# Kernel optimization log

Hardware: AMD Instinct MI355X
Metric: run time of the kernel (lower is better)

Reference implementation:

```python
import jax, jax.numpy as jnp
import numpy as np


def _ln(x, w, b, eps=1e-5):
    m = x.mean(-1, keepdims=True)
    v = jnp.mean((x - m) ** 2, axis=-1, keepdims=True)
    return (x - m) * jax.lax.rsqrt(v + eps) * w + b


def _to_seq(xc, g):
    # xc: [B,Di,H,W] -> [B,L,Di]; g0: row-major fwd, g1: row-major rev,
    # g2: col-major fwd, g3: col-major rev (CrossScan_1..4)
    if g >= 2:
        xc = xc.transpose(0, 1, 3, 2)
    s = xc.reshape(xc.shape[0], xc.shape[1], -1)
    if g % 2 == 1:
        s = jnp.flip(s, -1)
    return s.transpose(0, 2, 1)


def _from_seq(y, g, H, W):
    # y: [B,L,Di] -> [B,H,W,Di], inverse of _to_seq (CrossMerge_1..4)
    if g % 2 == 1:
        y = jnp.flip(y, 1)
    Bn, L, Di = y.shape
    if g >= 2:
        return y.reshape(Bn, W, H, Di).transpose(0, 2, 1, 3)
    return y.reshape(Bn, H, W, Di)


def _sscan(dA, dBx, Cm):
    # selective scan: h_t = dA_t*h + dBx_t ; y_t = <h_t, C_t>
    # dA,dBx: [B,L,Di,S], Cm: [B,L,S] -> y: [B,L,Di]
    def step(h, inp):
        a, bx, c = inp
        h = a * h + bx
        return h, jnp.einsum('bds,bs->bd', h, c)
    h0 = jnp.zeros(dA.shape[:1] + dA.shape[2:], dA.dtype)
    _, ys = jax.lax.scan(step, h0, (dA.transpose(1, 0, 2, 3), dBx.transpose(1, 0, 2, 3), Cm.transpose(1, 0, 2)))
    return ys.transpose(1, 0, 2)


def _ss2d(xc, g, H, W, ipw, ipb, cw, cb, xpw, dtw, dtb, A_log, Ds, onw, onb, opw, opb):
    R = dtw.shape[-1]
    S = A_log.shape[-1]
    xz = xc @ ipw.T + ipb                      # [B,H,W,2*Di]
    Di = xz.shape[-1] // 2
    xi, z = xz[..., :Di], xz[..., Di:]
    xi = xi.transpose(0, 3, 1, 2)              # [B,Di,H,W]
    xi = jax.lax.conv_general_dilated(xi, cw, (1, 1), [(1, 1), (1, 1)],
                                      dimension_numbers=('NCHW', 'OIHW', 'NCHW'),
                                      feature_group_count=Di) + cb[None, :, None, None]
    xi = jax.nn.silu(xi)
    seq = _to_seq(xi, g)                       # [B,L,Di]
    xdbl = seq @ xpw.T                         # [B,L,R+2S]
    dtr, Bm, Cm = xdbl[..., :R], xdbl[..., R:R + S], xdbl[..., R + S:]
    dt = jax.nn.softplus(dtr @ dtw.T + dtb)    # [B,L,Di]
    A = -jnp.exp(A_log)                        # [Di,S]
    dA = jnp.exp(dt[..., None] * A)            # [B,L,Di,S]
    dBx = (dt * seq)[..., None] * Bm[:, :, None, :]
    y = _sscan(dA, dBx, Cm) + Ds * seq
    y = _from_seq(y, g, H, W)                  # [B,H,W,Di]
    y = _ln(y, onw, onb)
    y = y * jax.nn.silu(z)
    return y @ opw.T + opb


def setup_inputs() -> dict:
    Bn, Hh, Ww, C = 8, 96, 96, 256
    Di = C // 4
    S = 1
    R = max(1, (Di + 15) // 16)
    key = jax.random.key(0)
    ks = jax.random.split(key, 12)
    nrm = lambda k, sh, s: jax.random.normal(k, sh, jnp.float32) * s
    return {
        'x': nrm(ks[0], (Bn, Hh * Ww, C), 1.0),
        'norm_w': jnp.ones((C,), jnp.float32), 'norm_b': jnp.zeros((C,), jnp.float32),
        'fc_w': nrm(ks[1], (C, C), 0.02), 'fc_b': jnp.zeros((C,), jnp.float32),
        'conv1d_w': nrm(ks[2], (1, 1, 3), 0.3),
        'in_proj_w': nrm(ks[3], (4, 2 * Di, Di), 0.05), 'in_proj_b': jnp.zeros((4, 2 * Di), jnp.float32),
        'conv2d_w': nrm(ks[4], (4, Di, 1, 3, 3), 0.2), 'conv2d_b': jnp.zeros((4, Di), jnp.float32),
        'x_proj_w': nrm(ks[5], (4, R + 2 * S, Di), 0.05),
        'dt_w': nrm(ks[6], (4, Di, R), 0.1), 'dt_b': nrm(ks[7], (4, Di), 0.1),
        'A_log': nrm(ks[8], (4, Di, S), 0.1),
        'Ds': jnp.ones((4, Di), jnp.float32),
        'out_norm_w': jnp.ones((4, Di), jnp.float32), 'out_norm_b': jnp.zeros((4, Di), jnp.float32),
        'out_proj_w': nrm(ks[9], (4, Di, Di), 0.05), 'out_proj_b': jnp.zeros((4, Di), jnp.float32),
        'proj_w': nrm(ks[10], (C, C), 0.02), 'proj_b': jnp.zeros((C,), jnp.float32),
        'skip_scale': jnp.ones((1,), jnp.float32),
        'H': Hh, 'W': Ww,
    }


def reference(x, norm_w, norm_b, fc_w, fc_b, conv1d_w, in_proj_w, in_proj_b, conv2d_w, conv2d_b,
              x_proj_w, dt_w, dt_b, A_log, Ds, out_norm_w, out_norm_b, out_proj_w, out_proj_b,
              proj_w, proj_b, skip_scale, H, W):
    B, N, C = x.shape
    xn = _ln(x, norm_w, norm_b)
    z_avg = xn.mean(1)                         # [B,C] (permute(0,2,1).mean(2))
    yg = jax.lax.conv_general_dilated(z_avg[:, None, :], conv1d_w, (1,), [(1, 1)],
                                      dimension_numbers=('NCH', 'OIH', 'NCH'))[:, 0, :]
    gate = jax.nn.sigmoid(z_avg @ fc_w.T + fc_b + yg)   # fc_out_2 [B,C]
    xg = xn.reshape(B, H, W, C)
    Dg = C // 4
    outs = [_ss2d(xg[..., g * Dg:(g + 1) * Dg], g, H, W,
                  in_proj_w[g], in_proj_b[g], conv2d_w[g], conv2d_b[g], x_proj_w[g],
                  dt_w[g], dt_b[g], A_log[g], Ds[g], out_norm_w[g], out_norm_b[g],
                  out_proj_w[g], out_proj_b[g]) for g in range(4)]
    xm = jnp.concatenate(outs, -1) * skip_scale * xg
    xm = xm.reshape(B, N, C) * gate[:, None, :]
    xm = _ln(xm, norm_w, norm_b)
    return xm @ proj_w.T + proj_b
```

## Files before the change

### kernel.cpp

```cpp
#include <hip/hip_runtime.h>
#include <math.h>

#define HH 96
#define WWI 96
#define NN 9216
#define CC 256
#define LL 9216
#define CHK 96
#define NCH 96
#define BB 8
#define BN (BB*NN)

__device__ __forceinline__ float softplusf(float x){
    float e = expf(-fabsf(x));
    return fmaxf(x, 0.f) + log1pf(e);
}
__device__ __forceinline__ float sigmf(float x){ return 1.f / (1.f + expf(-x)); }

__device__ __forceinline__ float wredsum(float v){
    #pragma unroll
    for(int o = 32; o > 0; o >>= 1) v += __shfl_xor(v, o, 64);
    return v;
}

__device__ __forceinline__ void wredsum2(float& s, float& q){
    #pragma unroll
    for(int o = 32; o > 0; o >>= 1){
        s += __shfl_xor(s, o, 64);
        q += __shfl_xor(q, o, 64);
    }
}

__device__ __forceinline__ void chunk_walk(int g, int chunk, int& base, int& step){
    if(g == 0){ base = chunk * 96;        step = 1;   }
    else if(g == 1){ base = 9215 - chunk * 96; step = -1; }
    else if(g == 2){ base = chunk;        step = 96;  }
    else { base = 9215 - chunk;           step = -96; }
}

__global__ __launch_bounds__(256) void k_stats(const float* __restrict__ x,
                                               float* __restrict__ mrs){
    int wid = threadIdx.x >> 6, lane = threadIdx.x & 63;
    size_t row = (size_t)blockIdx.x * 4 + wid;
    float4 v = ((const float4*)(x + row * CC))[lane];
    float s = wredsum(v.x + v.y + v.z + v.w);
    float q = wredsum(v.x*v.x + v.y*v.y + v.z*v.z + v.w*v.w);
    float m = s * (1.f/256.f);
    float var = q * (1.f/256.f) - m*m;
    float rs = rsqrtf(fmaxf(var, 0.f) + 1e-5f);
    if(lane == 0){ mrs[2*row] = m; mrs[2*row+1] = rs; }
}

__global__ __launch_bounds__(256) void k_prew(const float* __restrict__ pw,
        const float* __restrict__ nw, const float* __restrict__ nb,
        const float* __restrict__ pb, float* __restrict__ Wn,
        float* __restrict__ wsum, float* __restrict__ cvec){
    int o = threadIdx.x;
    float ws = 0.f, cc = 0.f;
    for(int k = 0; k < 256; k++){
        float w = pw[(size_t)o * 256 + k];
        float wn = w * nw[k];
        Wn[(size_t)o * 256 + k] = wn;
        ws += wn; cc += w * nb[k];
    }
    wsum[o] = ws; cvec[o] = cc + pb[o];
}

__global__ __launch_bounds__(128) void k_prewip(const float* __restrict__ ipw,
        const float* __restrict__ nw, const float* __restrict__ nb,
        const float* __restrict__ ipb, float* __restrict__ Wip,
        float* __restrict__ wsip, float* __restrict__ cvip){
    int g = blockIdx.x, o = threadIdx.x;
    const float* wr = ipw + ((size_t)(g*128 + o)) * 64;
    float ws = 0.f, cc = 0.f;
    for(int k = 0; k < 64; k++){
        float w = wr[k];
        float wn = w * nw[g*64 + k];
        Wip[((size_t)(g*128 + o))*64 + k] = wn;
        ws += wn; cc += w * nb[g*64 + k];
    }
    wsip[g*128 + o] = ws;
    cvip[g*128 + o] = cc + ipb[g*128 + o];
}

__global__ __launch_bounds__(256) void k_zavg(const float* __restrict__ x,
        const float* __restrict__ mrs, const float* __restrict__ nw,
        const float* __restrict__ nb, float* __restrict__ zpart){
    int c = threadIdx.x, b = blockIdx.y, t0 = blockIdx.x * 256;
    float nwv = nw[c], nbv = nb[c];
    float s = 0.f;
    for(int i = 0; i < 256; i++){
        size_t r = (size_t)b * NN + t0 + i;
        s += (x[r * CC + c] - mrs[2*r]) * mrs[2*r+1] * nwv + nbv;
    }
    zpart[((size_t)b * 36 + blockIdx.x) * CC + c] = s;
}

__global__ __launch_bounds__(256) void k_gate(const float* __restrict__ zpart,
        const float* __restrict__ fcw, const float* __restrict__ fcb,
        const float* __restrict__ w1d, float* __restrict__ gate){
    __shared__ float za[CC];
    int c = threadIdx.x, b = blockIdx.x;
    float s = 0.f;
    for(int t = 0; t < 36; t++) s += zpart[((size_t)b * 36 + t) * CC + c];
    za[c] = s * (1.f/(float)NN);
    __syncthreads();
    float zm1 = (c > 0)     ? za[c-1] : 0.f;
    float zp1 = (c < CC-1)  ? za[c+1] : 0.f;
    float acc = fcb[c] + w1d[0]*zm1 + w1d[1]*za[c] + w1d[2]*zp1;
    const float* wr = fcw + (size_t)c * CC;
    for(int k = 0; k < CC; k++) acc += za[k] * wr[k];
    gate[b * CC + c] = sigmf(acc);
}

__global__ __launch_bounds__(256) void k_inproj2(const float* __restrict__ x,
        const float* __restrict__ mrs, const float* __restrict__ Wip,
        const float* __restrict__ wsip, const float* __restrict__ cvip,
        float* __restrict__ xib, float* __restrict__ zbuf){
    int t = threadIdx.x;
    int g = blockIdx.y * 2 + (t >> 7);
    int h = (t >> 6) & 1;
    int c = t & 63;
    int r0 = blockIdx.x * 16;
    int b  = r0 / NN;
    int n0 = r0 - b * NN;
    int oc = g*128 + h*64 + c;
    float wv[64];
    {
        const float4* wr = (const float4*)(Wip + (size_t)oc * 64);
        #pragma unroll
        for(int j = 0; j < 16; j++){
            float4 t4 = wr[j];
            wv[4*j+0] = t4.x; wv[4*j+1] = t4.y;
            wv[4*j+2] = t4.z; wv[4*j+3] = t4.w;
        }
    }
    float acc[16];
    const float* ab = x + (size_t)r0 * CC + g * 64;
    #pragma unroll 4
    for(int r = 0; r < 16; r++){
        const float4* ar = (const float4*)(ab + (size_t)r * CC);
        float s0 = 0.f, s1 = 0.f;
        #pragma unroll
        for(int j = 0; j < 8; j++){
            float4 u = ar[j], v = ar[j + 8];
            s0 += u.x*wv[4*j+0]  + u.y*wv[4*j+1]  + u.z*wv[4*j+2]  + u.w*wv[4*j+3];
            s1 += v.x*wv[32+4*j] + v.y*wv[33+4*j] + v.z*wv[34+4*j] + v.w*wv[35+4*j];
        }
        acc[r] = s0 + s1;
    }
    float ws = wsip[oc], cv = cvip[oc];
    size_t obase = ((size_t)(b*4 + g)) * NN + n0;
    #pragma unroll
    for(int r = 0; r < 16; r++){
        size_t row = (size_t)r0 + r;
        float m = mrs[2*row], rs = mrs[2*row+1];
        float v = rs * acc[r] - m * rs * ws + cv;
        if(h == 0)
            xib[(obase + r)*64 + c] = v;
        else
            zbuf[(obase + r)*64 + c] = v * sigmf(v);
    }
}

__global__ __launch_bounds__(256) void k_inproj(const float* __restrict__ x,
        const float* __restrict__ mrs, const float* __restrict__ nw,
        const float* __restrict__ nb, const float* __restrict__ ipw,
        const float* __restrict__ ipb, float* __restrict__ xib,
        float* __restrict__ zbuf){
    int tile = blockIdx.x, b = blockIdx.y, g = blockIdx.z;
    int n0 = tile * 128;
    __shared__ float xs[128 * 64];
    int tid = threadIdx.x;
    for(int idx = tid; idx < 2048; idx += 256){
        int p = idx >> 4, k4 = (idx & 15) * 4;
        size_t r = (size_t)b * NN + n0 + p;
        float4 v = *(const float4*)(x + r * CC + g*64 + k4);
        float m = mrs[2*r], rs = mrs[2*r+1];
        float4 w4 = *(const float4*)(nw + g*64 + k4);
        float4 b4 = *(const float4*)(nb + g*64 + k4);
        float4 o;
        o.x = (v.x - m)*rs*w4.x + b4.x;
        o.y = (v.y - m)*rs*w4.y + b4.y;
        o.z = (v.z - m)*rs*w4.z + b4.z;
        o.w = (v.w - m)*rs*w4.w + b4.w;
        *(float4*)(xs + p*64 + k4) = o;
    }
    __syncthreads();
    int c = tid & 63, ph = tid >> 6;
    float wx[64], wz[64];
    {
        const float* wrx = ipw + ((size_t)(g*128 + c)) * 64;
        const float* wrz = ipw + ((size_t)(g*128 + 64 + c)) * 64;
        #pragma unroll
        for(int k = 0; k < 64; k++){ wx[k] = wrx[k]; wz[k] = wrz[k]; }
    }
    float bx = ipb[g*128 + c], bz = ipb[g*128 + 64 + c];
    size_t obase = ((size_t)(b*4 + g)) * NN + n0;
    for(int p = ph*32; p < ph*32 + 32; p++){
        const float4* xp = (const float4*)(xs + p*64);
        float a0 = 0.f, a1 = 0.f, z0 = 0.f, z1 = 0.f;
        #pragma unroll
        for(int k4 = 0; k4 < 16; k4 += 2){
            float4 u = xp[k4], v = xp[k4+1];
            a0 += u.x*wx[4*k4+0]; a1 += u.y*wx[4*k4+1];
            a0 += u.z*wx[4*k4+2]; a1 += u.w*wx[4*k4+3];
            z0 += u.x*wz[4*k4+0]; z1 += u.y*wz[4*k4+1];
            z0 += u.z*wz[4*k4+2]; z1 += u.w*wz[4*k4+3];
            a0 += v.x*wx[4*k4+4]; a1 += v.y*wx[4*k4+5];
            a0 += v.z*wx[4*k4+6]; a1 += v.w*wx[4*k4+7];
            z0 += v.x*wz[4*k4+4]; z1 += v.y*wz[4*k4+5];
            z0 += v.z*wz[4*k4+6]; z1 += v.w*wz[4*k4+7];
        }
        float xv = bx + a0 + a1;
        float zv = bz + z0 + z1;
        xib[(obase + p)*64 + c] = xv;
        zbuf[(obase + p)*64 + c] = zv * sigmf(zv);
    }
}

__global__ __launch_bounds__(256) void k_conv(const float* __restrict__ xib,
        const float* __restrict__ cw, const float* __restrict__ cb,
        float* __restrict__ out){
    int tile = blockIdx.x, b = blockIdx.y, g = blockIdx.z;
    int h0 = (tile/12)*8, w0 = (tile%12)*8;
    __shared__ float xs[100*64];
    int tid = threadIdx.x;
    size_t ibase = ((size_t)(b*4+g)) * NN;
    for(int i = tid; i < 6400; i += 256){
        int p = i >> 6, k = i & 63;
        int ph = h0 + p/10 - 1, pw = w0 + p%10 - 1;
        float v = 0.f;
        if(ph >= 0 && ph < HH && pw >= 0 && pw < WWI)
            v = xib[(ibase + (size_t)(ph*WWI + pw))*64 + k];
        xs[i] = v;
    }
    __syncthreads();
    int c = tid & 63, q = tid >> 6;
    float wk[9];
    const float* wp = cw + ((size_t)(g*64 + c))*9;
    #pragma unroll
    for(int j = 0; j < 9; j++) wk[j] = wp[j];
    float bias2 = cb[g*64 + c];
    for(int pi = q*16; pi < q*16+16; pi++){
        int py = pi >> 3, px = pi & 7;
        float acc = bias2;
        #pragma unroll
        for(int dy = 0; dy < 3; dy++)
            #pragma unroll
            for(int dx = 0; dx < 3; dx++)
                acc += xs[((py+dy)*10 + px+dx)*64 + c] * wk[dy*3+dx];
        float sv = acc * sigmf(acc);
        size_t r = (size_t)b*NN + (h0+py)*WWI + (w0+px);
        out[r*CC + g*64 + c] = sv;
    }
}

template<int ZPRE>
__global__ __launch_bounds__(256) void k_ipconv(const float* __restrict__ x,
        const float* __restrict__ mrs, const float* __restrict__ nw,
        const float* __restrict__ nb, const float* __restrict__ ipw,
        const float* __restrict__ ipb, const float* __restrict__ cw,
        const float* __restrict__ cb, float* __restrict__ out,
        float* __restrict__ zbuf){
    int tile = blockIdx.x, b = blockIdx.y, g = blockIdx.z;
    int h0 = (tile / 12) * 8, w0 = (tile % 12) * 8;
    __shared__ float xs[100 * 64];
    __shared__ float xi[100 * 64];
    int tid = threadIdx.x;
    for(int i = tid; i < 6400; i += 256){
        int p = i >> 6, k = i & 63;
        int ph = h0 + p / 10 - 1, pw = w0 + p % 10 - 1;
        float v = 0.f;
        if(ph >= 0 && ph < HH && pw >= 0 && pw < WWI){
            size_t r = (size_t)b * NN + ph * WWI + pw;
            v = (x[r * CC + g*64 + k] - mrs[2*r]) * mrs[2*r+1]
                * nw[g*64 + k] + nb[g*64 + k];
        }
        xs[i] = v;
    }
    __syncthreads();
    int c = tid & 63, q = tid >> 6;
    {
        float wv[64];
        const float* wr = ipw + ((size_t)(g * 128 + c)) * 64;
        #pragma unroll
        for(int k = 0; k < 64; k++) wv[k] = wr[k];
        float bias = ipb[g * 128 + c];
        for(int p = q * 25; p < q * 25 + 25; p++){
            int ph = h0 + p / 10 - 1, pw = w0 + p % 10 - 1;
            bool valid = (ph >= 0 && ph < HH && pw >= 0 && pw < WWI);
            float acc = bias;
            const float* xp = &xs[p * 64];
            #pragma unroll
            for(int k = 0; k < 64; k++) acc += xp[k] * wv[k];
            xi[p * 64 + c] = valid ? acc : 0.f;
        }
    }
    __syncthreads();
    float wk[9];
    const float* wp = cw + ((size_t)(g * 64 + c)) * 9;
    #pragma unroll
    for(int j = 0; j < 9; j++) wk[j] = wp[j];
    float bias2 = cb[g * 64 + c];
    for(int pi = q * 16; pi < q * 16 + 16; pi++){
        int py = pi >> 3, px = pi & 7;
        float acc = bias2;
        #pragma unroll
        for(int dy = 0; dy < 3; dy++)
            #pragma unroll
            for(int dx = 0; dx < 3; dx++)
                acc += xi[((py + dy) * 10 + px + dx) * 64 + c] * wk[dy*3 + dx];
        float sv = acc * sigmf(acc);
        size_t r = (size_t)b * NN + (h0 + py) * WWI + (w0 + px);
        out[r * CC + g*64 + c] = sv;
    }
    if(ZPRE){
        float wzv[64];
        const float* wr = ipw + ((size_t)(g * 128 + 64 + c)) * 64;
        #pragma unroll
        for(int k = 0; k < 64; k++) wzv[k] = wr[k];
        float zbv = ipb[g * 128 + 64 + c];
        size_t zb0 = ((size_t)(b * 4 + g)) * NN;
        for(int p16 = 0; p16 < 16; p16++){
            int p = q * 16 + p16;
            int py = p >> 3, px = p & 7;
            const float* xp = &xs[((py + 1) * 10 + (px + 1)) * 64];
            float acc = zbv;
            #pragma unroll
            for(int k = 0; k < 64; k++) acc += xp[k] * wzv[k];
            zbuf[(zb0 + (size_t)((h0 + py) * WWI + (w0 + px))) * 64 + c]
                = acc * sigmf(acc);
        }
    }
}

__global__ __launch_bounds__(64) void k_scan1(const float* __restrict__ out,
        const float* __restrict__ xpw, const float* __restrict__ dtw,
        const float* __restrict__ dtb, const float* __restrict__ alog,
        float* __restrict__ ap_out, float* __restrict__ h_out){
    int chunk = blockIdx.x, gb = blockIdx.y;
    int g = gb >> 3, b = gb & 7, d = threadIdx.x;
    __shared__ float s_seq[CHK * 65];
    __shared__ float s_xd[CHK * 6];
    __shared__ float s_w[6 * 64];
    int base, step; chunk_walk(g, chunk, base, step);
    const float* xg = out + (size_t)b * NN * CC + g * 64;
    for(int j = 0; j < CHK; j++)
        s_seq[j * 65 + d] = xg[(size_t)(base + j * step) * CC + d];
    for(int i = d; i < 384; i += 64) s_w[i] = xpw[g * 384 + i];
    __syncthreads();
    for(int idx = d; idx < CHK*6; idx += 64){
        int l = idx / 6, j = idx % 6;
        float acc = 0.f;
        const float* sr = &s_seq[l * 65];
        const float* wr = &s_w[j * 64];
        #pragma unroll
        for(int k = 0; k < 64; k++) acc += sr[k] * wr[k];
        s_xd[idx] = acc;
    }
    __syncthreads();
    int gd = g * 64 + d;
    float Av = -expf(alog[gd]);
    float db = dtb[gd];
    float w0 = dtw[gd*4], w1 = dtw[gd*4+1], w2 = dtw[gd*4+2], w3 = dtw[gd*4+3];
    float h = 0.f, apd = 1.f;
    #pragma unroll 4
    for(int l = 0; l < CHK; l++){
        const float* xd = &s_xd[l * 6];
        float xv = s_seq[l*65 + d];
        float dt = softplusf(xd[0]*w0 + xd[1]*w1 + xd[2]*w2 + xd[3]*w3 + db);
        float a = expf(dt * Av);
        h = a*h + dt*xv*xd[4];
        apd *= a;
    }
    int ob = (gb * NCH + chunk) * 64 + d;
    ap_out[ob] = apd; h_out[ob] = h;
}

__global__ __launch_bounds__(256) void k_scan2(const float* __restrict__ ap,
        const float* __restrict__ he, float* __restrict__ hinit){
    int idx = blockIdx.x * 256 + threadIdx.x;
    int gb = idx >> 6, d = idx & 63;
    float h = 0.f;
    for(int c = 0; c < NCH; c++){
        int o = (gb * NCH + c) * 64 + d;
        hinit[o] = h;
        h = ap[o]*h + he[o];
    }
}

template<int ZPRE>
__global__ __launch_bounds__(64) void k_scan3(float* __restrict__ out,
        const float* __restrict__ x, const float* __restrict__ mrs,
        const float* __restrict__ nw, const float* __restrict__ nb,
        const float* __restrict__ ipw, const float* __restrict__ ipb,
        const float* __restrict__ xpw, const float* __restrict__ dtw,
        const float* __restrict__ dtb, const float* __restrict__ alog,
        const float* __restrict__ Dsp, const float* __restrict__ onw,
        const float* __restrict__ onb, const float* __restrict__ hinit,
        const float* __restrict__ zbuf){
    int chunk = blockIdx.x, gb = blockIdx.y;
    int g = gb >> 3, b = gb & 7, d = threadIdx.x;
    __shared__ float s_seq[CHK * 65];
    __shared__ float s_xd[CHK * 6];
    __shared__ float s_w[6 * 64];
    __shared__ float xnt[(ZPRE ? 1 : CHK) * 65];
    int base, step; chunk_walk(g, chunk, base, step);
    float* xg = out + (size_t)b * NN * CC + g * 64;
    for(int j = 0; j < CHK; j++)
        s_seq[j * 65 + d] = xg[(size_t)(base + j * step) * CC + d];
    if(!ZPRE){
        float nwv = nw[g*64 + d], nbv = nb[g*64 + d];
        for(int j = 0; j < CHK; j++){
            int n = base + j * step;
            size_t r = (size_t)b * NN + n;
            xnt[j * 65 + d] = (x[r * CC + g*64 + d] - mrs[2*r]) * mrs[2*r+1] * nwv + nbv;
        }
    }
    for(int i = d; i < 384; i += 64) s_w[i] = xpw[g * 384 + i];
    __syncthreads();
    for(int idx = d; idx < CHK*6; idx += 64){
        int l = idx / 6, j = idx % 6;
        float acc = 0.f;
        const float* sr = &s_seq[l * 65];
        const float* wr = &s_w[j * 64];
        #pragma unroll
        for(int k = 0; k < 64; k++) acc += sr[k] * wr[k];
        s_xd[idx] = acc;
    }
    __syncthreads();
    int gd = g * 64 + d;
    float Av = -expf(alog[gd]);
    float db = dtb[gd];
    float Dv = Dsp[gd];
    float w0 = dtw[gd*4], w1 = dtw[gd*4+1], w2 = dtw[gd*4+2], w3 = dtw[gd*4+3];
    float h = hinit[(gb * NCH + chunk) * 64 + d];
    #pragma unroll 4
    for(int l = 0; l < CHK; l++){
        const float* xd = &s_xd[l * 6];
        float xv = s_seq[l*65 + d];
        float dt = softplusf(xd[0]*w0 + xd[1]*w1 + xd[2]*w2 + xd[3]*w3 + db);
        float a = expf(dt * Av);
        h = a*h + dt*xv*xd[4];
        s_seq[l*65 + d] = h * xd[5] + Dv * xv;
    }
    float wON = onw[gd], bON = onb[gd];
    float wz[ZPRE ? 1 : 64];
    float zb = 0.f;
    if(!ZPRE){
        const float* wr = ipw + ((size_t)(g * 128 + 64 + d)) * 64;
        #pragma unroll
        for(int k = 0; k < 64; k++) wz[k] = wr[k];
        zb = ipb[g * 128 + 64 + d];
    }
    const float* zp = zbuf + (((size_t)(b * 4 + g)) * NN) * 64 + d;
    #pragma unroll 4
    for(int l = 0; l < CHK; l++){
        float y = s_seq[l*65 + d];
        float s = y, q = y * y;
        wredsum2(s, q);
        float m = s * (1.f/64.f);
        float var = q * (1.f/64.f) - m*m;
        float rs = rsqrtf(fmaxf(var, 0.f) + 1e-5f);
        float lny = (y - m) * rs * wON + bON;
        int n = base + l * step;
        float zs;
        if(ZPRE){
            zs = zp[(size_t)n * 64];
        } else {
            float z = zb;
            const float* xp = &xnt[l * 65];
            #pragma unroll
            for(int k = 0; k < 64; k++) z += xp[k] * wz[k];
            zs = z * sigmf(z);
        }
        xg[(size_t)n * CC + d] = lny * zs;
    }
}

__global__ __launch_bounds__(64) void k_out2(float* __restrict__ out,
        const float* __restrict__ x, const float* __restrict__ mrs,
        const float* __restrict__ nw, const float* __restrict__ nb,
        const float* __restrict__ opw, const float* __restrict__ opb,
        const float* __restrict__ gate, const float* __restrict__ skip){
    int tile = blockIdx.x, b = blockIdx.y, g = blockIdx.z;
    int n0 = tile * 64, t = threadIdx.x;
    __shared__ float ly[64 * 65];
    __shared__ float xnt[64 * 65];
    float* xg = out + (size_t)b * NN * CC + g * 64;
    float nwv = nw[g*64 + t], nbv = nb[g*64 + t];
    for(int p = 0; p < 64; p++){
        size_t r = (size_t)b * NN + n0 + p;
        ly[p * 65 + t] = xg[(size_t)(n0 + p) * CC + t];
        xnt[p * 65 + t] = (x[r * CC + g*64 + t] - mrs[2*r]) * mrs[2*r+1] * nwv + nbv;
    }
    __syncthreads();
    float wv[64];
    const float* wr = opw + ((size_t)(g * 64 + t)) * 64;
    #pragma unroll
    for(int k = 0; k < 64; k++) wv[k] = wr[k];
    float bias = opb[g * 64 + t];
    float gv = gate[b * CC + g*64 + t];
    float sk = skip[0];
    for(int p = 0; p < 64; p++){
        float acc = bias;
        const float* yp = &ly[p * 65];
        #pragma unroll
        for(int k = 0; k < 64; k++) acc += yp[k] * wv[k];
        xg[(size_t)(n0 + p) * CC + t] = acc * sk * xnt[p * 65 + t] * gv;
    }
}

__global__ __launch_bounds__(256) void k_out3(const float* __restrict__ yin,
        const float* __restrict__ x, const float* __restrict__ mrs,
        const float* __restrict__ nw, const float* __restrict__ nb,
        const float* __restrict__ opw, const float* __restrict__ opb,
        const float* __restrict__ gate, const float* __restrict__ skip,
        float* __restrict__ zo, float* __restrict__ mrs2){
    __shared__ float ps[16 * 4], pq[16 * 4];
    int o = threadIdx.x;
    int g = o >> 6, c = o & 63;
    int r0 = blockIdx.x * 16;
    int b  = r0 / NN;
    int n0 = r0 - b * NN;
    float wv[64];
    {
        const float4* wr = (const float4*)(opw + ((size_t)(g*64 + c)) * 64);
        #pragma unroll
        for(int j = 0; j < 16; j++){
            float4 t4 = wr[j];
            wv[4*j+0] = t4.x; wv[4*j+1] = t4.y;
            wv[4*j+2] = t4.z; wv[4*j+3] = t4.w;
        }
    }
    float acc[16];
    const float* ab = yin + ((size_t)b * NN + n0) * CC + g * 64;
    #pragma unroll 4
    for(int r = 0; r < 16; r++){
        const float4* ar = (const float4*)(ab + (size_t)r * CC);
        float s0 = 0.f, s1 = 0.f;
        #pragma unroll
        for(int j = 0; j < 8; j++){
            float4 u = ar[j], v = ar[j + 8];
            s0 += u.x*wv[4*j+0]  + u.y*wv[4*j+1]  + u.z*wv[4*j+2]  + u.w*wv[4*j+3];
            s1 += v.x*wv[32+4*j] + v.y*wv[33+4*j] + v.z*wv[34+4*j] + v.w*wv[35+4*j];
        }
        acc[r] = s0 + s1;
    }
    float bias = opb[g*64 + c];
    float gv = gate[b * CC + g*64 + c];
    float sk = skip[0];
    float nwv = nw[g*64 + c], nbv = nb[g*64 + c];
    size_t zbase = ((size_t)(b*4 + g)) * NN + n0;
    #pragma unroll
    for(int r = 0; r < 16; r++){
        size_t row = (size_t)r0 + r;
        float xv = x[row * CC + g*64 + c];
        float xn = (xv - mrs[2*row]) * mrs[2*row+1] * nwv + nbv;
        float res = (acc[r] + bias) * sk * xn * gv;
        acc[r] = res;
        zo[(zbase + r) * 64 + c] = res;
    }
    #pragma unroll
    for(int r = 0; r < 16; r++){
        float s = acc[r], q = acc[r] * acc[r];
        wredsum2(s, q);
        if(c == 0){ ps[r*4 + g] = s; pq[r*4 + g] = q; }
    }
    __syncthreads();
    if(o < 16){
        float ss = ps[o*4] + ps[o*4+1] + ps[o*4+2] + ps[o*4+3];
        float qq = pq[o*4] + pq[o*4+1] + pq[o*4+2] + pq[o*4+3];
        float m = ss * (1.f/256.f);
        float var = qq * (1.f/256.f) - m*m;
        mrs2[2*((size_t)r0 + o)]     = m;
        mrs2[2*((size_t)r0 + o) + 1] = rsqrtf(fmaxf(var, 0.f) + 1e-5f);
    }
}

__global__ __launch_bounds__(256) void k_final(float* __restrict__ out,
        const float* __restrict__ nw, const float* __restrict__ nb,
        const float* __restrict__ pw, const float* __restrict__ pb){
    __shared__ float A[16 * 256];
    __shared__ float ps[256], pq[256];
    __shared__ float mrow[16], rrow[16];
    int n0 = blockIdx.x * 16;
    for(int i = threadIdx.x; i < 4096; i += 256)
        A[i] = out[(size_t)n0 * CC + i];
    __syncthreads();
    {
        int r = threadIdx.x >> 4, t16 = threadIdx.x & 15;
        float s = 0.f, q = 0.f;
        for(int j = 0; j < 16; j++){
            float v = A[r*256 + t16*16 + j];
            s += v; q += v*v;
        }
        ps[threadIdx.x] = s; pq[threadIdx.x] = q;
    }
    __syncthreads();
    if(threadIdx.x < 16){
        float ss = 0.f, qq = 0.f;
        for(int j = 0; j < 16; j++){ ss += ps[threadIdx.x*16 + j]; qq += pq[threadIdx.x*16 + j]; }
        float m = ss * (1.f/256.f);
        float var = qq * (1.f/256.f) - m*m;
        mrow[threadIdx.x] = m;
        rrow[threadIdx.x] = rsqrtf(fmaxf(var, 0.f) + 1e-5f);
    }
    __syncthreads();
    for(int i = threadIdx.x; i < 4096; i += 256){
        int r = i >> 8, c = i & 255;
        A[i] = (A[i] - mrow[r]) * rrow[r] * nw[c] + nb[c];
    }
    __syncthreads();
    int o = threadIdx.x;
    float acc[16];
    #pragma unroll
    for(int p = 0; p < 16; p++) acc[p] = 0.f;
    for(int kt = 0; kt < 4; kt++){
        float wv[64];
        const float4* wr = (const float4*)(pw + (size_t)o * CC + kt * 64);
        #pragma unroll
        for(int j = 0; j < 16; j++){
            float4 tq = wr[j];
            wv[4*j+0] = tq.x; wv[4*j+1] = tq.y;
            wv[4*j+2] = tq.z; wv[4*j+3] = tq.w;
        }
        #pragma unroll
        for(int p = 0; p < 16; p++){
            const float* ar = &A[p*256 + kt*64];
            float a = 0.f;
            #pragma unroll
            for(int k = 0; k < 64; k++) a += ar[k] * wv[k];
            acc[p] += a;
        }
    }
    float pbv = pb[o];
    #pragma unroll
    for(int p = 0; p < 16; p++)
        out[(size_t)(n0 + p) * CC + o] = acc[p] + pbv;
}

__global__ __launch_bounds__(256) void k_final2(const float* __restrict__ y,
        const float* __restrict__ mrs2, const float* __restrict__ Wn,
        const float* __restrict__ wsum, const float* __restrict__ cvec,
        float* __restrict__ out){
    int o = threadIdx.x;
    int r0 = blockIdx.x * 16;
    int b  = r0 / NN;
    int n0 = r0 - b * NN;
    float acc[16];
    #pragma unroll
    for(int r = 0; r < 16; r++) acc[r] = 0.f;
    for(int kt = 0; kt < 4; kt++){
        float wv[64];
        const float4* wr = (const float4*)(Wn + (size_t)o * 256 + kt * 64);
        #pragma unroll
        for(int j = 0; j < 16; j++){
            float4 t4 = wr[j];
            wv[4*j+0] = t4.x; wv[4*j+1] = t4.y;
            wv[4*j+2] = t4.z; wv[4*j+3] = t4.w;
        }
        const float* ab = y + ((size_t)(b*4 + kt)*NN + n0) * 64;
        #pragma unroll 4
        for(int r = 0; r < 16; r++){
            const float* ar = ab + (size_t)r * 64;
            float s0 = 0.f, s1 = 0.f;
            #pragma unroll
            for(int j = 0; j < 32; j++){
                s0 += ar[j]      * wv[j];
                s1 += ar[j + 32] * wv[j + 32];
            }
            acc[r] += s0 + s1;
        }
    }
    float wso = wsum[o], co = cvec[o];
    #pragma unroll
    for(int r = 0; r < 16; r++){
        float m  = mrs2[2*(size_t)(r0 + r)];
        float rs = mrs2[2*(size_t)(r0 + r) + 1];
        out[(size_t)(r0 + r) * CC + o] = rs * acc[r] - m * rs * wso + co;
    }
}

extern "C" void kernel_launch(void* const* d_in, const int* in_sizes, int n_in,
                              void* d_out, int out_size, void* d_ws, size_t ws_size,
                              hipStream_t stream){
    const float* x    = (const float*)d_in[0];
    const float* nw   = (const float*)d_in[1];
    const float* nb   = (const float*)d_in[2];
    const float* fcw  = (const float*)d_in[3];
    const float* fcb  = (const float*)d_in[4];
    const float* w1d  = (const float*)d_in[5];
    const float* ipw  = (const float*)d_in[6];
    const float* ipb  = (const float*)d_in[7];
    const float* cw   = (const float*)d_in[8];
    const float* cb   = (const float*)d_in[9];
    const float* xpw  = (const float*)d_in[10];
    const float* dtw  = (const float*)d_in[11];
    const float* dtb  = (const float*)d_in[12];
    const float* alog = (const float*)d_in[13];
    const float* Dsp  = (const float*)d_in[14];
    const float* onw  = (const float*)d_in[15];
    const float* onb  = (const float*)d_in[16];
    const float* opw  = (const float*)d_in[17];
    const float* opb  = (const float*)d_in[18];
    const float* pw   = (const float*)d_in[19];
    const float* pb   = (const float*)d_in[20];
    const float* skip = (const float*)d_in[21];

    char* base = (char*)d_ws;
    float* mrs  = (float*)base;
    float* gate = (float*)(base +  589824ull);
    float* ap   = (float*)(base +  598016ull);
    float* he   = (float*)(base + 1384448ull);
    float* hi   = (float*)(base + 2170880ull);
    float* zbuf = (float*)(base + 2957312ull);
    float* mrs2 = (float*)(base + 78454784ull);
    float* Wn   = (float*)(base + 79044608ull);
    float* wsum = (float*)(base + 79306752ull);
    float* cvec = (float*)(base + 79307776ull);
    float* xib  = (float*)(base + 79308800ull);
    float* Wip  = (float*)(base + 154806272ull);
    float* wsip = (float*)(base + 154937344ull);
    float* cvip = (float*)(base + 154939392ull);
    float* zpart = ap;
    float* out  = (float*)d_out;
    (void)in_sizes; (void)n_in; (void)out_size;

    const size_t T1 = 78454784ull;
    const size_t T2 = 79308800ull;
    const size_t T3 = 154806272ull;
    const size_t T4 = 154941440ull;
    bool usez    = ws_size >= T1;
    bool usef2   = ws_size >= T2;
    bool usesplit= ws_size >= T3;
    bool useip2  = ws_size >= T4;

    if(usef2)
        k_prew<<<1, 256, 0, stream>>>(pw, nw, nb, pb, Wn, wsum, cvec);
    if(useip2)
        k_prewip<<<4, 128, 0, stream>>>(ipw, nw, nb, ipb, Wip, wsip, cvip);
    k_stats <<<18432, 256, 0, stream>>>(x, mrs);
    k_zavg  <<<dim3(36, 8), 256, 0, stream>>>(x, mrs, nw, nb, zpart);
    k_gate  <<<8, 256, 0, stream>>>(zpart, fcw, fcb, w1d, gate);
    if(useip2){
        k_inproj2<<<dim3(4608, 2), 256, 0, stream>>>(x, mrs, Wip, wsip, cvip,
                                                     xib, zbuf);
        k_conv  <<<dim3(144, 8, 4), 256, 0, stream>>>(xib, cw, cb, out);
    } else if(usesplit){
        k_inproj<<<dim3(72, 8, 4), 256, 0, stream>>>(x, mrs, nw, nb, ipw, ipb,
                                                     xib, zbuf);
        k_conv  <<<dim3(144, 8, 4), 256, 0, stream>>>(xib, cw, cb, out);
    } else if(usez){
        k_ipconv<1><<<dim3(144, 8, 4), 256, 0, stream>>>(x, mrs, nw, nb, ipw, ipb,
                                                         cw, cb, out, zbuf);
    } else {
        k_ipconv<0><<<dim3(144, 8, 4), 256, 0, stream>>>(x, mrs, nw, nb, ipw, ipb,
                                                         cw, cb, out, zbuf);
    }
    k_scan1 <<<dim3(96, 32), 64, 0, stream>>>(out, xpw, dtw, dtb, alog, ap, he);
    k_scan2 <<<8, 256, 0, stream>>>(ap, he, hi);
    if(usez){
        k_scan3<1><<<dim3(96, 32), 64, 0, stream>>>(out, x, mrs, nw, nb, ipw, ipb,
                                                    xpw, dtw, dtb, alog, Dsp, onw,
                                                    onb, hi, zbuf);
    } else {
        k_scan3<0><<<dim3(96, 32), 64, 0, stream>>>(out, x, mrs, nw, nb, ipw, ipb,
                                                    xpw, dtw, dtb, alog, Dsp, onw,
                                                    onb, hi, zbuf);
    }
    if(usef2){
        k_out3  <<<4608, 256, 0, stream>>>(out, x, mrs, nw, nb, opw, opb,
                                           gate, skip, zbuf, mrs2);
        k_final2<<<4608, 256, 0, stream>>>(zbuf, mrs2, Wn, wsum, cvec, out);
    } else {
        k_out2  <<<dim3(144, 8, 4), 64, 0, stream>>>(out, x, mrs, nw, nb, opw, opb,
                                                     gate, skip);
        k_final <<<4608, 256, 0, stream>>>(out, nw, nb, pw, pb);
    }
}
```

Before: 1.348 ms.

## Rewrite in-projection kernel to read input rows through scalar loads

Replaces the in-projection kernel with one where each thread holds both the x-half and z-half weight rows in registers and walks 32 rows per wave. The wave-uniform activation rows and LayerNorm stats are fetched with inline-asm s_load_dwordx16 into SGPRs, so every lane reuses them without redundant vector loads. The grid is reorganised to tile/batch/group. This adds heavy register pressure (128 weight VGPRs plus 64 SGPRs) and serialises each load with a full lgkmcnt wait, leaving no overlap of loads with the FMAs.

```diff
diff --git a/kernel.cpp b/kernel.cpp
--- a/kernel.cpp
+++ b/kernel.cpp
@@ -1,5 +1,6 @@
 #include <hip/hip_runtime.h>
 #include <math.h>
+#include <stdint.h>
 
 #define HH 96
 #define WWI 96
@@ -11,6 +12,9 @@
 #define BB 8
 #define BN (BB*NN)
 
+typedef float f32x16 __attribute__((ext_vector_type(16)));
+typedef float f32x2  __attribute__((ext_vector_type(2)));
+
 __device__ __forceinline__ float softplusf(float x){
     float e = expf(-fabsf(x));
     return fmaxf(x, 0.f) + log1pf(e);
@@ -29,6 +33,13 @@
         s += __shfl_xor(s, o, 64);
         q += __shfl_xor(q, o, 64);
     }
+}
+
+__device__ __forceinline__ unsigned long long rfl64(const void* p){
+    unsigned long long a = (unsigned long long)(uintptr_t)p;
+    unsigned int lo = __builtin_amdgcn_readfirstlane((unsigned int)a);
+    unsigned int hi = __builtin_amdgcn_readfirstlane((unsigned int)(a >> 32));
+    return ((unsigned long long)hi << 32) | lo;
 }
 
 __device__ __forceinline__ void chunk_walk(int g, int chunk, int& base, int& step){
@@ -113,53 +124,60 @@
     gate[b * CC + c] = sigmf(acc);
 }
 
-__global__ __launch_bounds__(256) void k_inproj2(const float* __restrict__ x,
+__global__ __launch_bounds__(256) void k_inproj3(const float* __restrict__ x,
         const float* __restrict__ mrs, const float* __restrict__ Wip,
         const float* __restrict__ wsip, const float* __restrict__ cvip,
         float* __restrict__ xib, float* __restrict__ zbuf){
-    int t = threadIdx.x;
-    int g = blockIdx.y * 2 + (t >> 7);
-    int h = (t >> 6) & 1;
-    int c = t & 63;
-    int r0 = blockIdx.x * 16;
-    int b  = r0 / NN;
-    int n0 = r0 - b * NN;
-    int oc = g*128 + h*64 + c;
-    float wv[64];
+    int tile = blockIdx.x, b = blockIdx.y, g = blockIdx.z;
+    int n0 = tile * 128;
+    int c = threadIdx.x & 63, q = threadIdx.x >> 6;
+    float wx[64], wz[64];
     {
-        const float4* wr = (const float4*)(Wip + (size_t)oc * 64);
+        const float4* wrx = (const float4*)(Wip + ((size_t)(g*128 + c)) * 64);
+        const float4* wrz = (const float4*)(Wip + ((size_t)(g*128 + 64 + c)) * 64);
         #pragma unroll
         for(int j = 0; j < 16; j++){
-            float4 t4 = wr[j];
-            wv[4*j+0] = t4.x; wv[4*j+1] = t4.y;
-            wv[4*j+2] = t4.z; wv[4*j+3] = t4.w;
-        }
-    }
-    float acc[16];
-    const float* ab = x + (size_t)r0 * CC + g * 64;
-    #pragma unroll 4
-    for(int r = 0; r < 16; r++){
-        const float4* ar = (const float4*)(ab + (size_t)r * CC);
-        float s0 = 0.f, s1 = 0.f;
-        #pragma unroll
-        for(int j = 0; j < 8; j++){
-            float4 u = ar[j], v = ar[j + 8];
-            s0 += u.x*wv[4*j+0]  + u.y*wv[4*j+1]  + u.z*wv[4*j+2]  + u.w*wv[4*j+3];
-            s1 += v.x*wv[32+4*j] + v.y*wv[33+4*j] + v.z*wv[34+4*j] + v.w*wv[35+4*j];
-        }
-        acc[r] = s0 + s1;
-    }
-    float ws = wsip[oc], cv = cvip[oc];
-    size_t obase = ((size_t)(b*4 + g)) * NN + n0;
-    #pragma unroll
-    for(int r = 0; r < 16; r++){
-        size_t row = (size_t)r0 + r;
-        float m = mrs[2*row], rs = mrs[2*row+1];
-        float v = rs * acc[r] - m * rs * ws + cv;
-        if(h == 0)
-            xib[(obase + r)*64 + c] = v;
-        else
-            zbuf[(obase + r)*64 + c] = v * sigmf(v);
+            float4 u = wrx[j], v = wrz[j];
+            wx[4*j]=u.x; wx[4*j+1]=u.y; wx[4*j+2]=u.z; wx[4*j+3]=u.w;
+            wz[4*j]=v.x; wz[4*j+1]=v.y; wz[4*j+2]=v.z; wz[4*j+3]=v.w;
+        }
+    }
+    float wsx = wsip[g*128 + c],      cvx = cvip[g*128 + c];
+    float wsz = wsip[g*128 + 64 + c], cvz = cvip[g*128 + 64 + c];
+    size_t row0 = (size_t)b * NN + n0 + q*32;
+    unsigned long long xa0 = rfl64(x + row0 * CC + g*64);
+    unsigned long long ma0 = rfl64(mrs + 2 * row0);
+    size_t obase = ((size_t)(b*4 + g)) * NN + n0 + q*32;
+    for(int l = 0; l < 32; l++){
+        unsigned long long xa = xa0 + (unsigned long long)l * (CC*4);
+        unsigned long long ma = ma0 + (unsigned long long)l * 8;
+        f32x16 x0, x1, x2, x3; f32x2 mv;
+        asm volatile(
+            "s_load_dwordx16 %0, %5, 0x0\n\t"
+            "s_load_dwordx16 %1, %5, 0x40\n\t"
+            "s_load_dwordx16 %2, %5, 0x80\n\t"
+            "s_load_dwordx16 %3, %5, 0xc0\n\t"
+            "s_load_dwordx2  %4, %6, 0x0\n\t"
+            "s_waitcnt lgkmcnt(0)"
+            : "=s"(x0), "=s"(x1), "=s"(x2), "=s"(x3), "=s"(mv)
+            : "s"(xa), "s"(ma));
+        float ax0 = 0.f, ax1 = 0.f, az0 = 0.f, az1 = 0.f;
+        #pragma unroll
+        for(int k = 0; k < 16; k++){
+            ax0 += x0[k]*wx[k];     az0 += x0[k]*wz[k];
+            ax1 += x1[k]*wx[16+k];  az1 += x1[k]*wz[16+k];
+        }
+        #pragma unroll
+        for(int k = 0; k < 16; k++){
+            ax0 += x2[k]*wx[32+k];  az0 += x2[k]*wz[32+k];
+            ax1 += x3[k]*wx[48+k];  az1 += x3[k]*wz[48+k];
+        }
+        float m = mv[0], rv = mv[1];
+        float ax = ax0 + ax1, az = az0 + az1;
+        float vx = rv*ax - m*rv*wsx + cvx;
+        float vz = rv*az - m*rv*wsz + cvz;
+        xib [(obase + l)*64 + c] = vx;
+        zbuf[(obase + l)*64 + c] = vz * sigmf(vz);
     }
 }
 
@@ -735,18 +753,18 @@
     bool usez    = ws_size >= T1;
     bool usef2   = ws_size >= T2;
     bool usesplit= ws_size >= T3;
-    bool useip2  = ws_size >= T4;
+    bool useip3  = ws_size >= T4;
 
     if(usef2)
         k_prew<<<1, 256, 0, stream>>>(pw, nw, nb, pb, Wn, wsum, cvec);
-    if(useip2)
+    if(useip3)
         k_prewip<<<4, 128, 0, stream>>>(ipw, nw, nb, ipb, Wip, wsip, cvip);
     k_stats <<<18432, 256, 0, stream>>>(x, mrs);
     k_zavg  <<<dim3(36, 8), 256, 0, stream>>>(x, mrs, nw, nb, zpart);
     k_gate  <<<8, 256, 0, stream>>>(zpart, fcw, fcb, w1d, gate);
-    if(useip2){
-        k_inproj2<<<dim3(4608, 2), 256, 0, stream>>>(x, mrs, Wip, wsip, cvip,
-                                                     xib, zbuf);
+    if(useip3){
+        k_inproj3<<<dim3(72, 8, 4), 256, 0, stream>>>(x, mrs, Wip, wsip, cvip,
+                                                      xib, zbuf);
         k_conv  <<<dim3(144, 8, 4), 256, 0, stream>>>(xib, cw, cb, out);
     } else if(usesplit){
         k_inproj<<<dim3(72, 8, 4), 256, 0, stream>>>(x, mrs, nw, nb, ipw, ipb,
```

Result: faster. 1.118 ms (-17.0%).
